# Optimization experiments

Measured on AMD Instinct MI355X. Metric: run time of the kernel, lower is better.

The kernel has to match this reference:

```python
import jax, jax.numpy as jnp
import numpy as np

N, DN, DE, DOUT = 100000, 256, 128, 256
M1, B = 32768, 8192
E1, E2 = 10 * M1, 10 * B
DIN = DN + DN + DE  # self feats + (neighbor feats + edge feats)


def setup_inputs() -> dict:
    key = jax.random.key(0)
    ks = jax.random.split(key, 11)
    return {
        "node_features": jax.random.normal(ks[0], (N, DN), dtype=jnp.float32),
        "edge_feats1": jax.random.normal(ks[1], (E1, DE), dtype=jnp.float32),
        "edge_feats2": jax.random.normal(ks[2], (E2, DE), dtype=jnp.float32),
        "W1": jax.random.normal(ks[3], (DOUT, DIN), dtype=jnp.float32),
        "W2": jax.random.normal(ks[4], (DOUT, DIN), dtype=jnp.float32),
        "from_idx1": jax.random.randint(ks[5], (E1,), 0, N),
        "seg_idx1": jax.random.randint(ks[6], (E1,), 0, M1),
        "self_idx1": jax.random.randint(ks[7], (M1,), 0, N),
        "from_idx2": jax.random.randint(ks[8], (E2,), 0, N),
        "seg_idx2": jax.random.randint(ks[9], (E2,), 0, B),
        "self_idx2": jax.random.randint(ks[10], (B,), 0, M1),
    }


def _sage_layer(self_feats, agg_feats, W):
    # combined = cat([self, agg]); out = relu(W @ combined.T).T
    combined = jnp.concatenate([self_feats, agg_feats], axis=1)
    return jax.nn.relu(combined @ W.T)


def reference(node_features, edge_feats1, edge_feats2, W1, W2,
              from_idx1, seg_idx1, self_idx1, from_idx2, seg_idx2, self_idx2):
    m1 = self_idx1.shape[0]
    b = self_idx2.shape[0]
    # layer 1: aggregate over layer-0 -> layer-1 edges
    msg1 = jnp.concatenate([node_features[from_idx1], edge_feats1], axis=1)  # [E1, DN+DE]
    agg1 = jax.ops.segment_sum(msg1, seg_idx1, num_segments=m1)              # [M1, DN+DE]
    h1 = _sage_layer(node_features[self_idx1], agg1, W1)                     # [M1, DOUT]
    # layer 2: aggregate over layer-1 -> batch edges (from_states use raw node feats, as in torch)
    msg2 = jnp.concatenate([node_features[from_idx2], edge_feats2], axis=1)  # [E2, DN+DE]
    agg2 = jax.ops.segment_sum(msg2, seg_idx2, num_segments=b)               # [B, DN+DE]
    h2 = _sage_layer(h1[self_idx2], agg2, W2)                                # [B, DOUT]
    return h2
```

## Files before the change

kernel.cpp:

```cpp
#include <hip/hip_runtime.h>
#include <hip/hip_bf16.h>

#define N_NODES 100000
#define DN      256
#define DE      128
#define DOUT    256
#define M1      32768
#define BSZ     8192
#define E1      327680
#define E2      81920
#define DIN     640
#define DAGG    384
#define WELEMS  (DOUT * DIN)

#define CDIV(a,b) (((a)+(b)-1)/(b))

#define ZERO_INTS (M1 + BSZ + M1 + 64 + 256)
#define S1_ZB 73
#define S1_CB 80
#define S2_MB 8
#define S2_EB 400
#define GEMM1_BLOCKS 512

typedef __attribute__((ext_vector_type(8))) short bf16x8;
typedef __attribute__((ext_vector_type(4))) float f32x4;
typedef __attribute__((ext_vector_type(2))) float f32x2;
typedef __attribute__((ext_vector_type(4))) unsigned short u16x4;
typedef __attribute__((ext_vector_type(2))) unsigned short u16x2;

__device__ __forceinline__ unsigned short f32_bf16(float f) {
  unsigned u = __float_as_uint(f);
  unsigned r = (u + 0x7FFF + ((u >> 16) & 1)) >> 16;
  return (unsigned short)r;
}


__global__ __launch_bounds__(1024) void setup1_kernel(int* __restrict__ zbase,
                                                      const float* __restrict__ W1,
                                                      const float* __restrict__ W2,
                                                      unsigned short* __restrict__ Wb1,
                                                      unsigned short* __restrict__ Wb2) {
  int b = blockIdx.x, t = threadIdx.x;
  if (b < S1_ZB) {
    int i = b * 1024 + t;
    if (i < ZERO_INTS) zbase[i] = 0;
  } else {
    int i = ((b - S1_ZB) * 1024 + t) * 4;
    const float* s; unsigned short* d; int o;
    if (i < WELEMS) { s = W1; d = Wb1; o = i; }
    else { s = W2; d = Wb2; o = i - WELEMS; }
    f32x4 v = *reinterpret_cast<const f32x4*>(s + o);
    u16x4 r;
    r[0] = f32_bf16(v[0]); r[1] = f32_bf16(v[1]);
    r[2] = f32_bf16(v[2]); r[3] = f32_bf16(v[3]);
    *reinterpret_cast<u16x4*>(d + o) = r;
  }
}


__global__ __launch_bounds__(1024) void setup2_kernel(const int* __restrict__ self2,
                                                      int* __restrict__ claim,
                                                      const int* __restrict__ self1,
                                                      int* __restrict__ remap,
                                                      int* __restrict__ needed,
                                                      int* __restrict__ selfrow1,
                                                      int* __restrict__ nn,
                                                      const int* __restrict__ seg1,
                                                      const int* __restrict__ from1,
                                                      int* __restrict__ cnt1,
                                                      int2* __restrict__ bkt1,
                                                      const int* __restrict__ seg2,
                                                      const int* __restrict__ from2,
                                                      int* __restrict__ cnt2,
                                                      int2* __restrict__ bkt2) {
  int b = blockIdx.x, t = threadIdx.x;
  if (b < S2_MB) {
    int m = self2[b * 1024 + t];
    if (atomicCAS(&claim[m], 0, 1) == 0) {
      int p = atomicAdd(nn, 1);
      remap[m] = p;
      needed[p] = m;
      selfrow1[p] = self1[m];
    }
  } else {
    int e = (b - S2_MB) * 1024 + t;
    if (e < E1) {
      int s = seg1[e];
      int p = atomicAdd(&cnt1[s], 1);
      if (p < 64) bkt1[s * 64 + p] = make_int2(from1[e], e);
    } else {
      int e2 = e - E1;
      int s = seg2[e2];
      int p = atomicAdd(&cnt2[s], 1);
      if (p < 64) bkt2[s * 64 + p] = make_int2(from2[e2], e2);
    }
  }
}


__device__ __forceinline__ void agg_two_segments(int m0, bool v0, int m1, bool v1,
                                                 int r0, const int* __restrict__ cnt,
                                                 const int2* __restrict__ bkt,
                                                 const float* __restrict__ ef,
                                                 unsigned short* __restrict__ aggout,
                                                 const float* __restrict__ nf,
                                                 const float* __restrict__ zrow,
                                                 int l) {
  int mm[2] = {m0, m1};
  bool vv[2] = {v0, v1};
  int base_[2], nc_[2];
#pragma unroll
  for (int s = 0; s < 2; ++s) {
    nc_[s] = vv[s] ? min(cnt[mm[s]], 64) : 0;
    base_[s] = mm[s] * 64;
  }
  int eidp[2], fidp[2];
#pragma unroll
  for (int s = 0; s < 2; ++s) {
    eidp[s] = 0; fidp[s] = 0;
    if (l < nc_[s]) {
      int2 d = bkt[base_[s] + l];
      fidp[s] = d.x; eidp[s] = d.y;
    }
  }
  const float* zra = zrow + l * 4;
  const float* zrb = zrow + l * 2;

  f32x4 accn[2];
  f32x2 accf[2];
#pragma unroll
  for (int s = 0; s < 2; ++s) {
    accn[s] = (f32x4)0.f;
    accf[s] = (f32x2)0.f;
    int nc = nc_[s];
    int eid = eidp[s], fid = fidp[s];
    for (int j = 0; j < nc; j += 8) {
      f32x4 a[8]; f32x2 b[8];
#pragma unroll
      for (int q = 0; q < 8; ++q) {
        int jj = j + q;
        int fq = __shfl(fid, jj & 63);
        int gq = __shfl(eid, jj & 63);
        bool ok = jj < nc;
        const float* pa = ok ? (nf + (size_t)fq * 256 + l * 4) : zra;
        const float* pb = ok ? (ef + (size_t)gq * 128 + l * 2) : zrb;
        a[q] = *reinterpret_cast<const f32x4*>(pa);
        b[q] = *reinterpret_cast<const f32x2*>(pb);
      }
      accn[s] += ((a[0] + a[1]) + (a[2] + a[3])) + ((a[4] + a[5]) + (a[6] + a[7]));
      accf[s] += ((b[0] + b[1]) + (b[2] + b[3])) + ((b[4] + b[5]) + (b[6] + b[7]));
    }
  }

#pragma unroll
  for (int s = 0; s < 2; ++s) {
    unsigned short* orow = aggout + (size_t)(r0 + s) * DAGG;
    u16x4 on;
    on[0] = f32_bf16(accn[s][0]); on[1] = f32_bf16(accn[s][1]);
    on[2] = f32_bf16(accn[s][2]); on[3] = f32_bf16(accn[s][3]);
    *reinterpret_cast<u16x4*>(orow + l * 4) = on;
    u16x2 oe;
    oe[0] = f32_bf16(accf[s][0]); oe[1] = f32_bf16(accf[s][1]);
    *reinterpret_cast<u16x2*>(orow + 256 + l * 2) = oe;
  }
}


__global__ __launch_bounds__(256) void agg1_kernel(const int* __restrict__ needed,
                                                   const int* __restrict__ nn_dev,
                                                   const int* __restrict__ cnt1,
                                                   const int2* __restrict__ bkt1,
                                                   const float* __restrict__ ef1,
                                                   unsigned short* __restrict__ agg1,
                                                   const float* __restrict__ nf,
                                                   const float* __restrict__ zrow) {
  int wv = (blockIdx.x * 256 + threadIdx.x) >> 6;
  int l = threadIdx.x & 63;
  int s0 = wv * 2;
  int nnv = *nn_dev;
  bool v0 = s0 < nnv, v1 = (s0 + 1) < nnv;
  if (!v0) return;
  int m0 = needed[s0];
  int m1 = v1 ? needed[s0 + 1] : 0;
  agg_two_segments(m0, v0, m1, v1, s0, cnt1, bkt1, ef1, agg1, nf, zrow, l);
}


template<int MODE>
__device__ __forceinline__ void gemm_body(int bx, int by,
                                          const float* __restrict__ tabf,
                                          const unsigned short* __restrict__ tabb,
                                          const int* __restrict__ i1,
                                          const int* __restrict__ i2,
                                          const unsigned short* __restrict__ agg,
                                          const unsigned short* __restrict__ Wb,
                                          float* __restrict__ outf,
                                          unsigned short* __restrict__ outb,
                                          int nrows) {
  const int row0 = bx * 64;
  if (row0 >= nrows) return;
  const int col0 = by * 64;

  __shared__ unsigned short As[64][72];
  __shared__ unsigned short Bs[64][72];

  const int t = threadIdx.x;
  const int lane = t & 63, wid = t >> 6;
  const int wm = wid >> 1, wn = wid & 1;

  const int srow = t >> 2;
  const int scol = (t & 3) * 16;
  const int grow = row0 + srow;
  int ga = -1;
  if (grow < nrows) { int x = i1[grow]; ga = (MODE == 1) ? i2[x] : x; }
  const unsigned short* wrow = Wb + (size_t)(col0 + srow) * DIN + scol;
  const float* tabrow_f = (MODE == 0 && ga >= 0) ? tabf + (size_t)ga * 256 : nullptr;
  const unsigned short* tabrow_b = (MODE == 1 && ga >= 0) ? tabb + (size_t)ga * 256 : nullptr;
  const unsigned short* aggrow = agg + (size_t)grow * DAGG;

  f32x4 acc[2][2];
#pragma unroll
  for (int m = 0; m < 2; ++m)
#pragma unroll
    for (int n = 0; n < 2; ++n) acc[m][n] = (f32x4)0.f;

  bf16x8 ra0, ra1, rb0, rb1;

  auto loadA = [&](int k0, bf16x8& r0, bf16x8& r1) {
    int k = k0 + scol;
    if (ga < 0) { r0 = (bf16x8)(short)0; r1 = (bf16x8)(short)0; return; }
    if (k < 256) {
      if (MODE == 0) {
        const float* s = tabrow_f + k;
        f32x4 x0 = *reinterpret_cast<const f32x4*>(s);
        f32x4 x1 = *reinterpret_cast<const f32x4*>(s + 4);
        f32x4 x2 = *reinterpret_cast<const f32x4*>(s + 8);
        f32x4 x3 = *reinterpret_cast<const f32x4*>(s + 12);
#pragma unroll
        for (int j = 0; j < 4; ++j) {
          r0[j] = (short)f32_bf16(x0[j]); r0[4 + j] = (short)f32_bf16(x1[j]);
          r1[j] = (short)f32_bf16(x2[j]); r1[4 + j] = (short)f32_bf16(x3[j]);
        }
      } else {
        r0 = *reinterpret_cast<const bf16x8*>(tabrow_b + k);
        r1 = *reinterpret_cast<const bf16x8*>(tabrow_b + k + 8);
      }
    } else {
      r0 = *reinterpret_cast<const bf16x8*>(aggrow + (k - 256));
      r1 = *reinterpret_cast<const bf16x8*>(aggrow + (k - 256) + 8);
    }
  };

  loadA(0, ra0, ra1);
  rb0 = *reinterpret_cast<const bf16x8*>(wrow);
  rb1 = *reinterpret_cast<const bf16x8*>(wrow + 8);

  for (int k0 = 0; k0 < DIN; k0 += 64) {
    *reinterpret_cast<bf16x8*>(&As[srow][scol]) = ra0;
    *reinterpret_cast<bf16x8*>(&As[srow][scol + 8]) = ra1;
    *reinterpret_cast<bf16x8*>(&Bs[srow][scol]) = rb0;
    *reinterpret_cast<bf16x8*>(&Bs[srow][scol + 8]) = rb1;
    __syncthreads();

    if (k0 + 64 < DIN) {
      loadA(k0 + 64, ra0, ra1);
      rb0 = *reinterpret_cast<const bf16x8*>(wrow + k0 + 64);
      rb1 = *reinterpret_cast<const bf16x8*>(wrow + k0 + 64 + 8);
    }

#pragma unroll
    for (int ks = 0; ks < 2; ++ks) {
      bf16x8 af[2], bg[2];
#pragma unroll
      for (int m = 0; m < 2; ++m)
        af[m] = *reinterpret_cast<const bf16x8*>(
            &As[wm * 32 + m * 16 + (lane & 15)][ks * 32 + (lane >> 4) * 8]);
#pragma unroll
      for (int n = 0; n < 2; ++n)
        bg[n] = *reinterpret_cast<const bf16x8*>(
            &Bs[wn * 32 + n * 16 + (lane & 15)][ks * 32 + (lane >> 4) * 8]);
#pragma unroll
      for (int m = 0; m < 2; ++m)
#pragma unroll
        for (int n = 0; n < 2; ++n)
          acc[m][n] = __builtin_amdgcn_mfma_f32_16x16x32_bf16(af[m], bg[n], acc[m][n], 0, 0, 0);
    }
    __syncthreads();
  }

  const int rbase = row0 + wm * 32;
  const int cbase = col0 + wn * 32;
#pragma unroll
  for (int m = 0; m < 2; ++m)
#pragma unroll
    for (int n = 0; n < 2; ++n)
#pragma unroll
      for (int g = 0; g < 4; ++g) {
        int r = rbase + m * 16 + (lane >> 4) * 4 + g;
        if (r < nrows) {
          int c = cbase + n * 16 + (lane & 15);
          float x = fmaxf(acc[m][n][g], 0.f);
          if (MODE == 0) outb[(size_t)r * DOUT + c] = f32_bf16(x);
          else outf[(size_t)r * DOUT + c] = x;
        }
      }
}


__global__ __launch_bounds__(256, 4) void gemm1_agg2_kernel(const float* __restrict__ nf,
                                                            const int* __restrict__ selfrow1,
                                                            const unsigned short* __restrict__ agg1,
                                                            const unsigned short* __restrict__ Wb1,
                                                            unsigned short* __restrict__ h1c,
                                                            const int* __restrict__ nn_dev,
                                                            const int* __restrict__ cnt2,
                                                            const int2* __restrict__ bkt2,
                                                            const float* __restrict__ ef2,
                                                            unsigned short* __restrict__ agg2,
                                                            const float* __restrict__ zrow) {
  int b = blockIdx.x;
  if (b < GEMM1_BLOCKS) {
    gemm_body<0>(b >> 2, b & 3, nf, nullptr, selfrow1, nullptr, agg1, Wb1,
                 nullptr, h1c, *nn_dev);
  } else {
    int wv = ((b - GEMM1_BLOCKS) * 256 + threadIdx.x) >> 6;
    int l = threadIdx.x & 63;
    int s0 = wv * 2;
    agg_two_segments(s0, true, s0 + 1, true, s0, cnt2, bkt2, ef2, agg2,
                     nf, zrow, l);
  }
}


__global__ __launch_bounds__(256, 4) void gemm2_kernel(const unsigned short* __restrict__ h1c,
                                                       const int* __restrict__ self2,
                                                       const int* __restrict__ remap,
                                                       const unsigned short* __restrict__ agg2,
                                                       const unsigned short* __restrict__ Wb2,
                                                       float* __restrict__ out) {
  gemm_body<1>(blockIdx.x, blockIdx.y, nullptr, h1c, self2, remap, agg2, Wb2,
               out, nullptr, BSZ);
}


extern "C" void kernel_launch(void* const* d_in, const int* in_sizes, int n_in,
                              void* d_out, int out_size, void* d_ws, size_t ws_size,
                              hipStream_t stream) {
  const float* nf   = (const float*)d_in[0];
  const float* ef1  = (const float*)d_in[1];
  const float* ef2  = (const float*)d_in[2];
  const float* W1   = (const float*)d_in[3];
  const float* W2   = (const float*)d_in[4];
  const int* from1  = (const int*)d_in[5];
  const int* seg1   = (const int*)d_in[6];
  const int* self1  = (const int*)d_in[7];
  const int* from2  = (const int*)d_in[8];
  const int* seg2   = (const int*)d_in[9];
  const int* self2  = (const int*)d_in[10];
  float* out = (float*)d_out;

  char* w = (char*)d_ws;
  size_t o = 0;
  auto take = [&](size_t nb) -> char* {
    char* p = w + o;
    o += (nb + 255) & ~(size_t)255;
    return p;
  };
  int* cnt1 = (int*)take((size_t)M1 * 4);
  int* cnt2 = (int*)take((size_t)BSZ * 4);
  int* claim = (int*)take((size_t)M1 * 4);
  int* nn   = (int*)take(256);
  float* zrow = (float*)take((size_t)256 * 4);
  int* remap    = (int*)take((size_t)M1 * 4);
  int* needed   = (int*)take((size_t)8192 * 4);
  int* selfrow1 = (int*)take((size_t)8192 * 4);
  int2* bkt1    = (int2*)take((size_t)M1 * 64 * 8);
  int2* bkt2    = (int2*)take((size_t)BSZ * 64 * 8);
  unsigned short* Wb1   = (unsigned short*)take((size_t)WELEMS * 2);
  unsigned short* Wb2   = (unsigned short*)take((size_t)WELEMS * 2);
  unsigned short* agg1c = (unsigned short*)take((size_t)8192 * DAGG * 2);
  unsigned short* agg2  = (unsigned short*)take((size_t)8192 * DAGG * 2);
  unsigned short* h1c   = (unsigned short*)take((size_t)8192 * DOUT * 2);

  setup1_kernel<<<S1_ZB + S1_CB, 1024, 0, stream>>>((int*)d_ws, W1, W2, Wb1, Wb2);
  setup2_kernel<<<S2_MB + S2_EB, 1024, 0, stream>>>(self2, claim, self1, remap, needed,
                                                    selfrow1, nn,
                                                    seg1, from1, cnt1, bkt1,
                                                    seg2, from2, cnt2, bkt2);
  agg1_kernel<<<1024, 256, 0, stream>>>(needed, nn, cnt1, bkt1, ef1, agg1c, nf, zrow);
  gemm1_agg2_kernel<<<GEMM1_BLOCKS + 1024, 256, 0, stream>>>(nf, selfrow1, agg1c, Wb1,
                                                             h1c, nn,
                                                             cnt2, bkt2, ef2, agg2, zrow);
  gemm2_kernel<<<dim3(128, 4), 256, 0, stream>>>(h1c, self2, remap, agg2, Wb2, out);
}
```

Baseline: 90.12 us.

## Move E2 bucketing and weight conversion into the layer-1 aggregation kernel

Layer-2 edge bucketing and the bf16 weight conversion move out of the setup kernels and into extra blocks of the layer-1 aggregation launch. These steps do not depend on layer-1 results, so they can run alongside the memory-bound gather and shorten the serial setup phase. In exchange, the aggregation kernel becomes heterogeneous: its 256-thread blocks do three different jobs. The layer-2 bucket atomics may also contend with the aggregation traffic.

```diff
diff --git a/kernel.cpp b/kernel.cpp
--- a/kernel.cpp
+++ b/kernel.cpp
@@ -17,9 +17,11 @@
 
 #define ZERO_INTS (M1 + BSZ + M1 + 64 + 256)
 #define S1_ZB 73
-#define S1_CB 80
 #define S2_MB 8
-#define S2_EB 400
+#define S2_E1B 320
+#define L3_E2B 320
+#define L3_WB  320
+#define L3_AGG 1024
 #define GEMM1_BLOCKS 512
 
 typedef __attribute__((ext_vector_type(8))) short bf16x8;
@@ -35,44 +37,23 @@
 }
 
 
-__global__ __launch_bounds__(1024) void setup1_kernel(int* __restrict__ zbase,
-                                                      const float* __restrict__ W1,
-                                                      const float* __restrict__ W2,
-                                                      unsigned short* __restrict__ Wb1,
-                                                      unsigned short* __restrict__ Wb2) {
-  int b = blockIdx.x, t = threadIdx.x;
-  if (b < S1_ZB) {
-    int i = b * 1024 + t;
-    if (i < ZERO_INTS) zbase[i] = 0;
-  } else {
-    int i = ((b - S1_ZB) * 1024 + t) * 4;
-    const float* s; unsigned short* d; int o;
-    if (i < WELEMS) { s = W1; d = Wb1; o = i; }
-    else { s = W2; d = Wb2; o = i - WELEMS; }
-    f32x4 v = *reinterpret_cast<const f32x4*>(s + o);
-    u16x4 r;
-    r[0] = f32_bf16(v[0]); r[1] = f32_bf16(v[1]);
-    r[2] = f32_bf16(v[2]); r[3] = f32_bf16(v[3]);
-    *reinterpret_cast<u16x4*>(d + o) = r;
-  }
-}
-
-
-__global__ __launch_bounds__(1024) void setup2_kernel(const int* __restrict__ self2,
-                                                      int* __restrict__ claim,
-                                                      const int* __restrict__ self1,
-                                                      int* __restrict__ remap,
-                                                      int* __restrict__ needed,
-                                                      int* __restrict__ selfrow1,
-                                                      int* __restrict__ nn,
-                                                      const int* __restrict__ seg1,
-                                                      const int* __restrict__ from1,
-                                                      int* __restrict__ cnt1,
-                                                      int2* __restrict__ bkt1,
-                                                      const int* __restrict__ seg2,
-                                                      const int* __restrict__ from2,
-                                                      int* __restrict__ cnt2,
-                                                      int2* __restrict__ bkt2) {
+__global__ __launch_bounds__(1024) void setup1_kernel(int* __restrict__ zbase) {
+  int i = blockIdx.x * 1024 + threadIdx.x;
+  if (i < ZERO_INTS) zbase[i] = 0;
+}
+
+
+__global__ __launch_bounds__(1024) void setup2a_kernel(const int* __restrict__ self2,
+                                                       int* __restrict__ claim,
+                                                       const int* __restrict__ self1,
+                                                       int* __restrict__ remap,
+                                                       int* __restrict__ needed,
+                                                       int* __restrict__ selfrow1,
+                                                       int* __restrict__ nn,
+                                                       const int* __restrict__ seg1,
+                                                       const int* __restrict__ from1,
+                                                       int* __restrict__ cnt1,
+                                                       int2* __restrict__ bkt1) {
   int b = blockIdx.x, t = threadIdx.x;
   if (b < S2_MB) {
     int m = self2[b * 1024 + t];
@@ -84,16 +65,9 @@
     }
   } else {
     int e = (b - S2_MB) * 1024 + t;
-    if (e < E1) {
-      int s = seg1[e];
-      int p = atomicAdd(&cnt1[s], 1);
-      if (p < 64) bkt1[s * 64 + p] = make_int2(from1[e], e);
-    } else {
-      int e2 = e - E1;
-      int s = seg2[e2];
-      int p = atomicAdd(&cnt2[s], 1);
-      if (p < 64) bkt2[s * 64 + p] = make_int2(from2[e2], e2);
-    }
+    int s = seg1[e];
+    int p = atomicAdd(&cnt1[s], 1);
+    if (p < 64) bkt1[s * 64 + p] = make_int2(from1[e], e);
   }
 }
 
@@ -166,23 +140,49 @@
 }
 
 
-__global__ __launch_bounds__(256) void agg1_kernel(const int* __restrict__ needed,
-                                                   const int* __restrict__ nn_dev,
-                                                   const int* __restrict__ cnt1,
-                                                   const int2* __restrict__ bkt1,
-                                                   const float* __restrict__ ef1,
-                                                   unsigned short* __restrict__ agg1,
-                                                   const float* __restrict__ nf,
-                                                   const float* __restrict__ zrow) {
-  int wv = (blockIdx.x * 256 + threadIdx.x) >> 6;
-  int l = threadIdx.x & 63;
-  int s0 = wv * 2;
-  int nnv = *nn_dev;
-  bool v0 = s0 < nnv, v1 = (s0 + 1) < nnv;
-  if (!v0) return;
-  int m0 = needed[s0];
-  int m1 = v1 ? needed[s0 + 1] : 0;
-  agg_two_segments(m0, v0, m1, v1, s0, cnt1, bkt1, ef1, agg1, nf, zrow, l);
+__global__ __launch_bounds__(256) void agg1mix_kernel(const int* __restrict__ seg2,
+                                                      const int* __restrict__ from2,
+                                                      int* __restrict__ cnt2,
+                                                      int2* __restrict__ bkt2,
+                                                      const float* __restrict__ W1,
+                                                      const float* __restrict__ W2,
+                                                      unsigned short* __restrict__ Wb1,
+                                                      unsigned short* __restrict__ Wb2,
+                                                      const int* __restrict__ needed,
+                                                      const int* __restrict__ nn_dev,
+                                                      const int* __restrict__ cnt1,
+                                                      const int2* __restrict__ bkt1,
+                                                      const float* __restrict__ ef1,
+                                                      unsigned short* __restrict__ agg1,
+                                                      const float* __restrict__ nf,
+                                                      const float* __restrict__ zrow) {
+  int b = blockIdx.x, t = threadIdx.x;
+  if (b < L3_E2B) {
+    int e2 = b * 256 + t;
+    int s = seg2[e2];
+    int p = atomicAdd(&cnt2[s], 1);
+    if (p < 64) bkt2[s * 64 + p] = make_int2(from2[e2], e2);
+  } else if (b < L3_E2B + L3_WB) {
+    int i = ((b - L3_E2B) * 256 + t) * 4;
+    const float* s; unsigned short* d; int o;
+    if (i < WELEMS) { s = W1; d = Wb1; o = i; }
+    else { s = W2; d = Wb2; o = i - WELEMS; }
+    f32x4 v = *reinterpret_cast<const f32x4*>(s + o);
+    u16x4 r;
+    r[0] = f32_bf16(v[0]); r[1] = f32_bf16(v[1]);
+    r[2] = f32_bf16(v[2]); r[3] = f32_bf16(v[3]);
+    *reinterpret_cast<u16x4*>(d + o) = r;
+  } else {
+    int wv = ((b - L3_E2B - L3_WB) * 256 + t) >> 6;
+    int l = t & 63;
+    int s0 = wv * 2;
+    int nnv = *nn_dev;
+    bool v0 = s0 < nnv, v1 = (s0 + 1) < nnv;
+    if (!v0) return;
+    int m0 = needed[s0];
+    int m1 = v1 ? needed[s0 + 1] : 0;
+    agg_two_segments(m0, v0, m1, v1, s0, cnt1, bkt1, ef1, agg1, nf, zrow, l);
+  }
 }
 
 
@@ -382,12 +382,14 @@
   unsigned short* agg2  = (unsigned short*)take((size_t)8192 * DAGG * 2);
   unsigned short* h1c   = (unsigned short*)take((size_t)8192 * DOUT * 2);
 
-  setup1_kernel<<<S1_ZB + S1_CB, 1024, 0, stream>>>((int*)d_ws, W1, W2, Wb1, Wb2);
-  setup2_kernel<<<S2_MB + S2_EB, 1024, 0, stream>>>(self2, claim, self1, remap, needed,
-                                                    selfrow1, nn,
-                                                    seg1, from1, cnt1, bkt1,
-                                                    seg2, from2, cnt2, bkt2);
-  agg1_kernel<<<1024, 256, 0, stream>>>(needed, nn, cnt1, bkt1, ef1, agg1c, nf, zrow);
+  setup1_kernel<<<S1_ZB, 1024, 0, stream>>>((int*)d_ws);
+  setup2a_kernel<<<S2_MB + S2_E1B, 1024, 0, stream>>>(self2, claim, self1, remap, needed,
+                                                      selfrow1, nn,
+                                                      seg1, from1, cnt1, bkt1);
+  agg1mix_kernel<<<L3_E2B + L3_WB + L3_AGG, 256, 0, stream>>>(seg2, from2, cnt2, bkt2,
+                                                              W1, W2, Wb1, Wb2,
+                                                              needed, nn, cnt1, bkt1,
+                                                              ef1, agg1c, nf, zrow);
   gemm1_agg2_kernel<<<GEMM1_BLOCKS + 1024, 256, 0, stream>>>(nf, selfrow1, agg1c, Wb1,
                                                              h1c, nn,
                                                              cnt2, bkt2, ef2, agg2, zrow);
```

New measurement: 89.65 us. Within noise of the previous version (-0.5%).
